# Optimization experiments

Hardware: AMD Instinct MI355X
Metric: run time of the kernel (lower is better)

Reference implementation:

```python
import jax, jax.numpy as jnp
import numpy as np

B, CIN, COUT, K, L = 16, 512, 512, 3, 8192
STRIDE, PAD, DIL = 1, 1, 1  # 'same' conv: Lout == L


def setup_inputs() -> dict:
    key = jax.random.key(0)
    k1, k2, k3 = jax.random.split(key, 3)
    x = jax.random.normal(k1, (B, CIN, L), dtype=jnp.float32)
    # int8 quantized weight stored as int32 for portability; values in [-128, 127]
    qweight = jax.random.randint(k2, (COUT, CIN, K), -128, 128, dtype=jnp.int32)
    scale = jnp.float32(0.01)  # per-tensor dequant scale (w_max / 127)
    bias = jax.random.normal(k3, (COUT,), dtype=jnp.float32)
    return {"x": x, "qweight": qweight, "scale": scale, "bias": bias}


def reference(x, qweight, scale, bias):
    # Dequantize: fp32 weight = int8 * scale (materialized every call, as in torch module)
    w = (qweight.astype(jnp.float32) * scale).astype(x.dtype)
    out = jax.lax.conv_general_dilated(
        x, w,
        window_strides=(STRIDE,),
        padding=[(PAD, PAD)],
        rhs_dilation=(DIL,),
        dimension_numbers=("NCH", "OIH", "NCH"),
        feature_group_count=1,
    )
    return out + bias.astype(x.dtype)[None, :, None]
```

## Files before the change

kernel.cpp:

```cpp
#include <hip/hip_runtime.h>
#include <hip/hip_bf16.h>

#define CIN   512
#define COUT  512
#define LEN   8192
#define NB    16
#define KW    3
#define PROWS 8200

#define WB_ELEMS (COUT * CIN * KW)
#define WB_BYTES ((size_t)WB_ELEMS * 2)
#define XS_BYTES ((size_t)NB * PROWS * CIN * 2)

#define XPREP_BLOCKS (NB * 8 * (LEN / 64))
#define WCONV_BLOCKS ((WB_ELEMS + 255) / 256)

#define BM2 256
#define BN2 256
#define BK3 64
#define NT  24
#define TILE3 (BM2 * BK3 * 2)

typedef __attribute__((ext_vector_type(4)))  float f32x4;
typedef __attribute__((ext_vector_type(16))) float f32x16;
typedef __attribute__((ext_vector_type(8)))  short bf16x8;

static __device__ __forceinline__ unsigned short f2bf(float f) {
    union { float f; unsigned u; } cv; cv.f = f;
    return (unsigned short)((cv.u + 0x7fffu + ((cv.u >> 16) & 1u)) >> 16);
}

__global__ __launch_bounds__(256) void prep_kernel(const float* __restrict__ x,
                                                   const int* __restrict__ q,
                                                   unsigned short* __restrict__ xs,
                                                   unsigned short* __restrict__ wb) {
    __shared__ char T[64 * 132];
    int blk = blockIdx.x;
    int tid = threadIdx.x;

    if (blk >= XPREP_BLOCKS) {
        int idx = (blk - XPREP_BLOCKS) * 256 + tid;
        if (idx < WB_ELEMS) {
            int co = idx / (KW * CIN);
            int r  = idx - co * (KW * CIN);
            int t  = r >> 9;
            int ci = r & 511;
            wb[idx] = f2bf((float)q[(co * CIN + ci) * KW + t]);
        }
        return;
    }

    int b   = blk >> 10;
    int ci0 = ((blk >> 7) & 7) * 64;
    int l0  = (blk & 127) * 64;

    if (l0 == 0 && tid < 64)
        xs[((size_t)b * PROWS + 0) * CIN + ci0 + tid] = 0;
    if (l0 == (LEN - 64) && tid < 64)
        xs[((size_t)b * PROWS + (LEN + 1)) * CIN + ci0 + tid] = 0;

    const float* src = x + ((size_t)b * CIN + ci0) * LEN + l0;
    for (int i = tid; i < 64 * 16; i += 256) {
        int r = i >> 4, c4 = i & 15;
        f32x4 v = *(const f32x4*)(src + (size_t)r * LEN + c4 * 4);
        unsigned lo = (unsigned)f2bf(v[0]) | ((unsigned)f2bf(v[1]) << 16);
        unsigned hi = (unsigned)f2bf(v[2]) | ((unsigned)f2bf(v[3]) << 16);
        char* p = T + r * 132 + c4 * 8;
        *(unsigned*)p       = lo;
        *(unsigned*)(p + 4) = hi;
    }
    __syncthreads();
    unsigned short* dst = xs + ((size_t)b * PROWS + 1 + l0) * CIN + ci0;
    for (int i = tid; i < 64 * 8; i += 256) {
        int l = i >> 3, c8 = i & 7;
        union { bf16x8 v; unsigned short s[8]; } pk;
        #pragma unroll
        for (int j = 0; j < 8; ++j)
            pk.s[j] = *(const unsigned short*)(T + (c8 * 8 + j) * 132 + l * 2);
        *(bf16x8*)(dst + (size_t)l * CIN + c8 * 8) = pk.v;
    }
}

__global__ __launch_bounds__(512, 2) void conv_kernel(
    const unsigned short* __restrict__ xs,
    const unsigned short* __restrict__ wb,
    const float* __restrict__ scale_p,
    const float* __restrict__ bias,
    float* __restrict__ out)
{
    __shared__ char sA[2][TILE3];
    __shared__ char sB[2][TILE3];

    const int bid = blockIdx.x;
    const int logical = (bid & 7) * 128 + (bid >> 3);
    const int co_tile = logical & 1;
    const int l_tile  = logical >> 1;
    const int b   = l_tile >> 5;
    const int l0  = (l_tile & 31) * BN2;
    const int co0 = co_tile * BM2;

    const int tid  = threadIdx.x;
    const int lane = tid & 63;
    const int wid  = tid >> 6;
    const int wr   = wid >> 2;
    const int wc   = wid & 3;
    const int la   = lane & 31;
    const int lh   = lane >> 5;

    f32x16 acc[4][2] = {};

    const char* xsB = (const char*)(xs + ((size_t)b * PROWS + l0) * CIN);
    const char* wbB = (const char*)wb + (size_t)co0 * (KW * CIN * 2);

#define STAGEU(buf_, c_, u_) do {                                                            \
    int tap_ = (c_) % KW;  int ci0_ = ((c_) / KW) * BK3;                                     \
    int rowoff_ = ((u_) & 1) * 128;                                                          \
    const char* src0_; size_t rstride_; char* dst0_;                                         \
    if ((u_) < 2) { src0_ = xsB + ((size_t)(tap_ + rowoff_) * CIN + ci0_) * 2;               \
                    rstride_ = CIN * 2; dst0_ = &sB[buf_][rowoff_ * 128]; }                   \
    else          { src0_ = wbB + (size_t)rowoff_ * (KW * CIN * 2)                           \
                            + ((size_t)tap_ * CIN + ci0_) * 2;                               \
                    rstride_ = KW * CIN * 2; dst0_ = &sA[buf_][rowoff_ * 128]; }             \
    _Pragma("unroll")                                                                        \
    for (int kk_ = 0; kk_ < 2; ++kk_) {                                                      \
        int it_ = tid + kk_ * 512;                                                           \
        int r_ = it_ >> 3, q_ = it_ & 7;                                                     \
        __builtin_amdgcn_global_load_lds(                                                    \
            (const __attribute__((address_space(1))) unsigned int*)                          \
                (src0_ + (size_t)r_ * rstride_ + ((q_ * 16) ^ ((r_ & 7) << 4))),             \
            (__attribute__((address_space(3))) unsigned int*)(dst0_ + it_ * 16),             \
            16, 0, 0);                                                                       \
    } } while (0)

#define LDA(d_, buf_, mb_, s_) do { int row_ = (mb_) * 64 + wr * 32 + la;                    \
    d_ = *(const bf16x8*)(&sA[buf_][0] + row_ * 128                                          \
                          + (((s_) * 32 + lh * 16) ^ ((row_ & 7) << 4))); } while (0)
#define LDB(d_, buf_, nb_, s_) do { int row_ = wc * 64 + (nb_) * 32 + la;                    \
    d_ = *(const bf16x8*)(&sB[buf_][0] + row_ * 128                                          \
                          + (((s_) * 32 + lh * 16) ^ ((row_ & 7) << 4))); } while (0)

#define MFMA8(MB_, B00_, B01_, B10_, B11_) do {                                              \
    __builtin_amdgcn_s_setprio(1);                                                           \
    acc[(MB_)  ][0] = __builtin_amdgcn_mfma_f32_32x32x16_bf16(a0_, B00_, acc[(MB_)  ][0],0,0,0); \
    acc[(MB_)  ][1] = __builtin_amdgcn_mfma_f32_32x32x16_bf16(a0_, B01_, acc[(MB_)  ][1],0,0,0); \
    acc[(MB_)+1][0] = __builtin_amdgcn_mfma_f32_32x32x16_bf16(a2_, B00_, acc[(MB_)+1][0],0,0,0); \
    acc[(MB_)+1][1] = __builtin_amdgcn_mfma_f32_32x32x16_bf16(a2_, B01_, acc[(MB_)+1][1],0,0,0); \
    acc[(MB_)  ][0] = __builtin_amdgcn_mfma_f32_32x32x16_bf16(a1_, B10_, acc[(MB_)  ][0],0,0,0); \
    acc[(MB_)  ][1] = __builtin_amdgcn_mfma_f32_32x32x16_bf16(a1_, B11_, acc[(MB_)  ][1],0,0,0); \
    acc[(MB_)+1][0] = __builtin_amdgcn_mfma_f32_32x32x16_bf16(a3_, B10_, acc[(MB_)+1][0],0,0,0); \
    acc[(MB_)+1][1] = __builtin_amdgcn_mfma_f32_32x32x16_bf16(a3_, B11_, acc[(MB_)+1][1],0,0,0); \
    __builtin_amdgcn_s_setprio(0);                                                           \
    } while (0)

#define BAR()    __builtin_amdgcn_s_barrier()
#define SCHED0() __builtin_amdgcn_sched_barrier(0)
#define LGKM0()  asm volatile("s_waitcnt lgkmcnt(0)" ::: "memory")

    STAGEU(0, 0, 0); STAGEU(0, 0, 1); STAGEU(0, 0, 2); STAGEU(0, 0, 3);
    asm volatile("s_waitcnt vmcnt(2)" ::: "memory");
    BAR();

    bf16x8 b00, b01, b10, b11, b20, b21, b30, b31;
    bf16x8 a0_, a1_, a2_, a3_;

    #pragma unroll 1
    for (int c = 0; c < NT - 1; ++c) {
        const int buf = c & 1, nb = buf ^ 1;
        SCHED0();
        LDB(b00, buf, 0, 0); LDB(b01, buf, 1, 0);
        LDB(b10, buf, 0, 1); LDB(b11, buf, 1, 1);
        LDB(b20, buf, 0, 2); LDB(b21, buf, 1, 2);
        LDB(b30, buf, 0, 3); LDB(b31, buf, 1, 3);
        LDA(a0_, buf, 0, 0); LDA(a1_, buf, 0, 1); LDA(a2_, buf, 1, 0); LDA(a3_, buf, 1, 1);
        STAGEU(nb, c + 1, 0);
        BAR(); LGKM0(); SCHED0();
        MFMA8(0, b00, b01, b10, b11);
        SCHED0();
        LDA(a0_, buf, 0, 2); LDA(a1_, buf, 0, 3); LDA(a2_, buf, 1, 2); LDA(a3_, buf, 1, 3);
        STAGEU(nb, c + 1, 1);
        asm volatile("s_waitcnt vmcnt(4)" ::: "memory");
        BAR(); LGKM0(); SCHED0();
        MFMA8(0, b20, b21, b30, b31);
        SCHED0();
        LDA(a0_, buf, 2, 0); LDA(a1_, buf, 2, 1); LDA(a2_, buf, 3, 0); LDA(a3_, buf, 3, 1);
        STAGEU(nb, c + 1, 2);
        BAR(); LGKM0(); SCHED0();
        MFMA8(2, b00, b01, b10, b11);
        SCHED0();
        LDA(a0_, buf, 2, 2); LDA(a1_, buf, 2, 3); LDA(a2_, buf, 3, 2); LDA(a3_, buf, 3, 3);
        STAGEU(nb, c + 1, 3);
        asm volatile("s_waitcnt vmcnt(2)" ::: "memory");
        BAR(); LGKM0(); SCHED0();
        MFMA8(2, b20, b21, b30, b31);
    }
    {
        const int buf = (NT - 1) & 1;
        SCHED0();
        LDB(b00, buf, 0, 0); LDB(b01, buf, 1, 0);
        LDB(b10, buf, 0, 1); LDB(b11, buf, 1, 1);
        LDB(b20, buf, 0, 2); LDB(b21, buf, 1, 2);
        LDB(b30, buf, 0, 3); LDB(b31, buf, 1, 3);
        LDA(a0_, buf, 0, 0); LDA(a1_, buf, 0, 1); LDA(a2_, buf, 1, 0); LDA(a3_, buf, 1, 1);
        BAR(); LGKM0(); SCHED0();
        MFMA8(0, b00, b01, b10, b11);
        SCHED0();
        LDA(a0_, buf, 0, 2); LDA(a1_, buf, 0, 3); LDA(a2_, buf, 1, 2); LDA(a3_, buf, 1, 3);
        asm volatile("s_waitcnt vmcnt(0)" ::: "memory");
        BAR(); LGKM0(); SCHED0();
        MFMA8(0, b20, b21, b30, b31);
        SCHED0();
        LDA(a0_, buf, 2, 0); LDA(a1_, buf, 2, 1); LDA(a2_, buf, 3, 0); LDA(a3_, buf, 3, 1);
        BAR(); LGKM0(); SCHED0();
        MFMA8(2, b00, b01, b10, b11);
        SCHED0();
        LDA(a0_, buf, 2, 2); LDA(a1_, buf, 2, 3); LDA(a2_, buf, 3, 2); LDA(a3_, buf, 3, 3);
        LGKM0(); SCHED0();
        MFMA8(2, b20, b21, b30, b31);
    }
#undef STAGEU
#undef LDA
#undef LDB
#undef MFMA8

    const float sc = scale_p[0];
    #pragma unroll
    for (int mb = 0; mb < 4; ++mb) {
        const int coB = co0 + mb * 64 + wr * 32 + 4 * lh;
        #pragma unroll
        for (int rg = 0; rg < 16; ++rg) {
            int co = coB + (rg & 3) + 8 * (rg >> 2);
            float bv = bias[co];
            size_t orow = ((size_t)b * COUT + co) * LEN + l0 + wc * 64 + la;
            out[orow]      = sc * acc[mb][0][rg] + bv;
            out[orow + 32] = sc * acc[mb][1][rg] + bv;
        }
    }
}

__global__ __launch_bounds__(256) void wconv_kernel(const int* __restrict__ q,
                                                    unsigned short* __restrict__ wb) {
    int idx = blockIdx.x * 256 + threadIdx.x;
    if (idx >= WB_ELEMS) return;
    int co = idx / (KW * CIN);
    int r  = idx - co * (KW * CIN);
    int t  = r >> 9;
    int ci = r & 511;
    wb[idx] = f2bf((float)q[(co * CIN + ci) * KW + t]);
}

__global__ __launch_bounds__(256, 2) void conv_fb_kernel(
    const float* __restrict__ x,
    const unsigned short* __restrict__ wb,
    const float* __restrict__ scale_p,
    const float* __restrict__ bias,
    float* __restrict__ out)
{
    __shared__ char xT[132 * 128];
    const int bid = blockIdx.x;
    const int logical = (bid & 7) * 512 + (bid >> 3);
    const int co_tile = logical & 3;
    const int n_tile  = logical >> 2;
    const int b   = n_tile >> 6;
    const int l0  = (n_tile & 63) * 128;
    const int co0 = co_tile * 128;
    const int tid  = threadIdx.x;
    const int lane = tid & 63;
    const int wid  = tid >> 6;
    const int wr = wid >> 1, wc = wid & 1;
    const int lhi = lane >> 4;
    const int llo = lane & 15;
    f32x4 acc[4][4] = {};
    const float* xb = x + (size_t)b * CIN * LEN;

    for (int ci0 = 0; ci0 < CIN; ci0 += 64) {
        __syncthreads();
        for (int it = tid; it < 132 * 8; it += 256) {
            int c = it % 132;
            int o = it / 132;
            int l = l0 - 1 + c;
            float v[8];
            if (l >= 0 && l < LEN) {
                const float* src = xb + (size_t)(ci0 + o * 8) * LEN + l;
                #pragma unroll
                for (int j = 0; j < 8; ++j) v[j] = src[(size_t)j * LEN];
            } else {
                #pragma unroll
                for (int j = 0; j < 8; ++j) v[j] = 0.f;
            }
            union { bf16x8 v8; unsigned short s[8]; } pk;
            #pragma unroll
            for (int j = 0; j < 8; ++j) pk.s[j] = f2bf(v[j]);
            int byte = c * 128 + ((o * 16) ^ ((c & 7) << 4));
            *reinterpret_cast<bf16x8*>(xT + byte) = pk.v8;
        }
        __syncthreads();
        #pragma unroll
        for (int t = 0; t < KW; ++t) {
            #pragma unroll
            for (int s = 0; s < 2; ++s) {
                bf16x8 af[4];
                #pragma unroll
                for (int m = 0; m < 4; ++m)
                    af[m] = *reinterpret_cast<const bf16x8*>(
                        wb + (size_t)(co0 + wr * 64 + m * 16 + llo) * (KW * CIN)
                           + t * CIN + ci0 + s * 32 + 8 * lhi);
                bf16x8 bfr[4];
                #pragma unroll
                for (int n = 0; n < 4; ++n) {
                    int col = wc * 64 + n * 16 + llo + t;
                    int byte = col * 128 + (((s * 32 + 8 * lhi) * 2) ^ ((col & 7) << 4));
                    bfr[n] = *reinterpret_cast<const bf16x8*>(xT + byte);
                }
                #pragma unroll
                for (int m = 0; m < 4; ++m)
                    #pragma unroll
                    for (int n = 0; n < 4; ++n)
                        acc[m][n] = __builtin_amdgcn_mfma_f32_16x16x32_bf16(af[m], bfr[n], acc[m][n], 0, 0, 0);
            }
        }
    }
    const float sc = scale_p[0];
    #pragma unroll
    for (int m = 0; m < 4; ++m) {
        #pragma unroll
        for (int j = 0; j < 4; ++j) {
            int co = co0 + wr * 64 + m * 16 + lhi * 4 + j;
            float bv = bias[co];
            size_t orow = ((size_t)b * COUT + co) * LEN + l0 + wc * 64;
            #pragma unroll
            for (int n = 0; n < 4; ++n)
                out[orow + n * 16 + llo] = sc * acc[m][n][j] + bv;
        }
    }
}

extern "C" void kernel_launch(void* const* d_in, const int* in_sizes, int n_in,
                              void* d_out, int out_size, void* d_ws, size_t ws_size,
                              hipStream_t stream) {
    const float* x    = (const float*)d_in[0];
    const int*   qw   = (const int*)d_in[1];
    const float* sc   = (const float*)d_in[2];
    const float* bias = (const float*)d_in[3];
    float* out = (float*)d_out;
    unsigned short* wb = (unsigned short*)d_ws;

    if (ws_size >= WB_BYTES + XS_BYTES) {
        unsigned short* xsw = (unsigned short*)((char*)d_ws + WB_BYTES);
        prep_kernel<<<XPREP_BLOCKS + WCONV_BLOCKS, 256, 0, stream>>>(x, qw, xsw, wb);
        conv_kernel<<<(COUT / BM2) * (NB * LEN / BN2), 512, 0, stream>>>(xsw, wb, sc, bias, out);
    } else {
        wconv_kernel<<<WCONV_BLOCKS, 256, 0, stream>>>(qw, wb);
        conv_fb_kernel<<<4096, 256, 0, stream>>>(x, wb, sc, bias, out);
    }
}
```

Before: 296.4 us.

## Repack activations and weights into 8-channel planes matching LDS fragment layout

```diff
diff --git a/kernel.cpp b/kernel.cpp
--- a/kernel.cpp
+++ b/kernel.cpp
@@ -10,7 +10,8 @@
 
 #define WB_ELEMS (COUT * CIN * KW)
 #define WB_BYTES ((size_t)WB_ELEMS * 2)
-#define XS_BYTES ((size_t)NB * PROWS * CIN * 2)
+#define PLANEB   ((size_t)PROWS * 16)
+#define XS_BYTES ((size_t)NB * 8 * 8 * PLANEB)
 
 #define XPREP_BLOCKS (NB * 8 * (LEN / 64))
 #define WCONV_BLOCKS ((WB_ELEMS + 255) / 256)
@@ -19,7 +20,6 @@
 #define BN2 256
 #define BK3 64
 #define NT  24
-#define TILE3 (BM2 * BK3 * 2)
 
 typedef __attribute__((ext_vector_type(4)))  float f32x4;
 typedef __attribute__((ext_vector_type(16))) float f32x16;
@@ -32,8 +32,8 @@
 
 __global__ __launch_bounds__(256) void prep_kernel(const float* __restrict__ x,
                                                    const int* __restrict__ q,
-                                                   unsigned short* __restrict__ xs,
-                                                   unsigned short* __restrict__ wb) {
+                                                   char* __restrict__ xs2,
+                                                   char* __restrict__ wb2) {
     __shared__ char T[64 * 132];
     int blk = blockIdx.x;
     int tid = threadIdx.x;
@@ -41,25 +41,35 @@
     if (blk >= XPREP_BLOCKS) {
         int idx = (blk - XPREP_BLOCKS) * 256 + tid;
         if (idx < WB_ELEMS) {
-            int co = idx / (KW * CIN);
-            int r  = idx - co * (KW * CIN);
-            int t  = r >> 9;
-            int ci = r & 511;
-            wb[idx] = f2bf((float)q[(co * CIN + ci) * KW + t]);
+            int co  = idx / (CIN * KW);
+            int rem = idx - co * (CIN * KW);
+            int ci  = rem / KW;
+            int t   = rem - ci * KW;
+            unsigned short v = f2bf((float)q[idx]);
+            int cc = (ci >> 6) * KW + t;
+            size_t byte = ((size_t)(co >> 8) * NT + cc) * 32768
+                        + (size_t)((ci >> 3) & 7) * 4096
+                        + (size_t)(co & 255) * 16 + (ci & 7) * 2;
+            *(unsigned short*)(wb2 + byte) = v;
         }
         return;
     }
 
     int b   = blk >> 10;
-    int ci0 = ((blk >> 7) & 7) * 64;
+    int q8  = (blk >> 7) & 7;
     int l0  = (blk & 127) * 64;
-
-    if (l0 == 0 && tid < 64)
-        xs[((size_t)b * PROWS + 0) * CIN + ci0 + tid] = 0;
-    if (l0 == (LEN - 64) && tid < 64)
-        xs[((size_t)b * PROWS + (LEN + 1)) * CIN + ci0 + tid] = 0;
-
-    const float* src = x + ((size_t)b * CIN + ci0) * LEN + l0;
+    char* xp = xs2 + ((size_t)(b * 8 + q8) * 8) * PLANEB;
+
+    if (l0 == 0 && tid < 8) {
+        f32x4 z = {};
+        *(f32x4*)(xp + (size_t)tid * PLANEB) = z;
+    }
+    if (l0 == (LEN - 64) && tid < 8) {
+        f32x4 z = {};
+        *(f32x4*)(xp + (size_t)tid * PLANEB + (size_t)(LEN + 1) * 16) = z;
+    }
+
+    const float* src = x + ((size_t)b * CIN + q8 * 64) * LEN + l0;
     for (int i = tid; i < 64 * 16; i += 256) {
         int r = i >> 4, c4 = i & 15;
         f32x4 v = *(const f32x4*)(src + (size_t)r * LEN + c4 * 4);
@@ -70,26 +80,25 @@
         *(unsigned*)(p + 4) = hi;
     }
     __syncthreads();
-    unsigned short* dst = xs + ((size_t)b * PROWS + 1 + l0) * CIN + ci0;
     for (int i = tid; i < 64 * 8; i += 256) {
         int l = i >> 3, c8 = i & 7;
         union { bf16x8 v; unsigned short s[8]; } pk;
         #pragma unroll
         for (int j = 0; j < 8; ++j)
             pk.s[j] = *(const unsigned short*)(T + (c8 * 8 + j) * 132 + l * 2);
-        *(bf16x8*)(dst + (size_t)l * CIN + c8 * 8) = pk.v;
+        *(bf16x8*)(xp + (size_t)c8 * PLANEB + (size_t)(1 + l0 + l) * 16) = pk.v;
     }
 }
 
 __global__ __launch_bounds__(512, 2) void conv_kernel(
-    const unsigned short* __restrict__ xs,
-    const unsigned short* __restrict__ wb,
+    const char* __restrict__ xs2,
+    const char* __restrict__ wb2,
     const float* __restrict__ scale_p,
     const float* __restrict__ bias,
     float* __restrict__ out)
 {
-    __shared__ char sA[2][TILE3];
-    __shared__ char sB[2][TILE3];
+    __shared__ char sA[2][32768];
+    __shared__ char sB[2][32768];
 
     const int bid = blockIdx.x;
     const int logical = (bid & 7) * 128 + (bid >> 3);
@@ -109,35 +118,38 @@
 
     f32x16 acc[4][2] = {};
 
-    const char* xsB = (const char*)(xs + ((size_t)b * PROWS + l0) * CIN);
-    const char* wbB = (const char*)wb + (size_t)co0 * (KW * CIN * 2);
+    const char* wbA  = wb2 + (size_t)co_tile * NT * 32768;
+    const char* xs2b = xs2 + (size_t)b * 8 * 8 * PLANEB + (size_t)l0 * 16;
+
+    const int ldsW = wid * 4096 + lane * 16;
+    const size_t bS0 = (size_t)wid * PLANEB + lane * 16;
+
+    const char* pAr = &sA[0][0] + lh * 4096 + wr * 512 + la * 16;
+    const char* pBr = &sB[0][0] + lh * 4096 + wc * 1024 + la * 16;
+
+#define BAR()    __builtin_amdgcn_s_barrier()
+#define SCHED0() __builtin_amdgcn_sched_barrier(0)
+#define LGKM0()  asm volatile("s_waitcnt lgkmcnt(0)" ::: "memory")
+
+#define GL(src_, dst_) __builtin_amdgcn_global_load_lds(                                     \
+    (const __attribute__((address_space(1))) unsigned int*)(src_),                           \
+    (__attribute__((address_space(3))) unsigned int*)(dst_), 16, 0, 0)
 
 #define STAGEU(buf_, c_, u_) do {                                                            \
-    int tap_ = (c_) % KW;  int ci0_ = ((c_) / KW) * BK3;                                     \
-    int rowoff_ = ((u_) & 1) * 128;                                                          \
-    const char* src0_; size_t rstride_; char* dst0_;                                         \
-    if ((u_) < 2) { src0_ = xsB + ((size_t)(tap_ + rowoff_) * CIN + ci0_) * 2;               \
-                    rstride_ = CIN * 2; dst0_ = &sB[buf_][rowoff_ * 128]; }                   \
-    else          { src0_ = wbB + (size_t)rowoff_ * (KW * CIN * 2)                           \
-                            + ((size_t)tap_ * CIN + ci0_) * 2;                               \
-                    rstride_ = KW * CIN * 2; dst0_ = &sA[buf_][rowoff_ * 128]; }             \
-    _Pragma("unroll")                                                                        \
-    for (int kk_ = 0; kk_ < 2; ++kk_) {                                                      \
-        int it_ = tid + kk_ * 512;                                                           \
-        int r_ = it_ >> 3, q_ = it_ & 7;                                                     \
-        __builtin_amdgcn_global_load_lds(                                                    \
-            (const __attribute__((address_space(1))) unsigned int*)                          \
-                (src0_ + (size_t)r_ * rstride_ + ((q_ * 16) ^ ((r_ & 7) << 4))),             \
-            (__attribute__((address_space(3))) unsigned int*)(dst0_ + it_ * 16),             \
-            16, 0, 0);                                                                       \
+    int tap_ = (c_) % KW;  int q_ = (c_) / KW;                                               \
+    if ((u_) < 2) {                                                                          \
+        const char* s_ = xs2b + (size_t)q_ * (8 * PLANEB) + bS0                              \
+                         + (size_t)(tap_ + (u_) * 128) * 16;                                 \
+        char* d_ = &sB[buf_][0] + ldsW + (u_) * 2048;                                        \
+        GL(s_, d_);  GL(s_ + 1024, d_ + 1024);                                               \
+    } else {                                                                                 \
+        const char* s_ = wbA + (size_t)(c_) * 32768 + ldsW + ((u_) & 1) * 2048;              \
+        char* d_ = &sA[buf_][0] + ldsW + ((u_) & 1) * 2048;                                  \
+        GL(s_, d_);  GL(s_ + 1024, d_ + 1024);                                               \
     } } while (0)
 
-#define LDA(d_, buf_, mb_, s_) do { int row_ = (mb_) * 64 + wr * 32 + la;                    \
-    d_ = *(const bf16x8*)(&sA[buf_][0] + row_ * 128                                          \
-                          + (((s_) * 32 + lh * 16) ^ ((row_ & 7) << 4))); } while (0)
-#define LDB(d_, buf_, nb_, s_) do { int row_ = wc * 64 + (nb_) * 32 + la;                    \
-    d_ = *(const bf16x8*)(&sB[buf_][0] + row_ * 128                                          \
-                          + (((s_) * 32 + lh * 16) ^ ((row_ & 7) << 4))); } while (0)
+#define LDA(d_, buf_, mb_, s_) d_ = *(const bf16x8*)(pAr + (buf_) * 32768 + (s_) * 8192 + (mb_) * 1024)
+#define LDB(d_, buf_, nb_, s_) d_ = *(const bf16x8*)(pBr + (buf_) * 32768 + (s_) * 8192 + (nb_) * 512)
 
 #define MFMA8(MB_, B00_, B01_, B10_, B11_) do {                                              \
     __builtin_amdgcn_s_setprio(1);                                                           \
@@ -152,10 +164,6 @@
     __builtin_amdgcn_s_setprio(0);                                                           \
     } while (0)
 
-#define BAR()    __builtin_amdgcn_s_barrier()
-#define SCHED0() __builtin_amdgcn_sched_barrier(0)
-#define LGKM0()  asm volatile("s_waitcnt lgkmcnt(0)" ::: "memory")
-
     STAGEU(0, 0, 0); STAGEU(0, 0, 1); STAGEU(0, 0, 2); STAGEU(0, 0, 3);
     asm volatile("s_waitcnt vmcnt(2)" ::: "memory");
     BAR();
@@ -221,6 +229,7 @@
 #undef LDA
 #undef LDB
 #undef MFMA8
+#undef GL
 
     const float sc = scale_p[0];
     #pragma unroll
@@ -342,13 +351,14 @@
     const float* sc   = (const float*)d_in[2];
     const float* bias = (const float*)d_in[3];
     float* out = (float*)d_out;
-    unsigned short* wb = (unsigned short*)d_ws;
 
     if (ws_size >= WB_BYTES + XS_BYTES) {
-        unsigned short* xsw = (unsigned short*)((char*)d_ws + WB_BYTES);
-        prep_kernel<<<XPREP_BLOCKS + WCONV_BLOCKS, 256, 0, stream>>>(x, qw, xsw, wb);
-        conv_kernel<<<(COUT / BM2) * (NB * LEN / BN2), 512, 0, stream>>>(xsw, wb, sc, bias, out);
+        char* wb2 = (char*)d_ws;
+        char* xs2 = (char*)d_ws + WB_BYTES;
+        prep_kernel<<<XPREP_BLOCKS + WCONV_BLOCKS, 256, 0, stream>>>(x, qw, xs2, wb2);
+        conv_kernel<<<(COUT / BM2) * (NB * LEN / BN2), 512, 0, stream>>>(xs2, wb2, sc, bias, out);
     } else {
+        unsigned short* wb = (unsigned short*)d_ws;
         wconv_kernel<<<WCONV_BLOCKS, 256, 0, stream>>>(qw, wb);
         conv_fb_kernel<<<4096, 256, 0, stream>>>(x, wb, sc, bias, out);
     }
```

Measured after the change: 298.6 us. About the same (+0.7%).
